# Kernel tuning notes

Measured on AMD Instinct MI355X. Metric: run time of the kernel, lower is better.

## Reference

```python
import jax, jax.numpy as jnp
import numpy as np

N_NODES = 100000
N_EDGES = 1600000
D_IN = 128
D_HID = 128
D_OUT = 2
N_GRAPHS = 64


def setup_inputs() -> dict:
    key = jax.random.key(0)
    ks = jax.random.split(key, 10)
    x = jax.random.normal(ks[0], (N_NODES, D_IN), dtype=jnp.float32)
    edge_index = jax.random.randint(ks[1], (2, N_EDGES), 0, N_NODES, dtype=jnp.int64)
    batch = jnp.sort(jax.random.randint(ks[2], (N_NODES,), 0, N_GRAPHS, dtype=jnp.int64))
    s_in = 1.0 / np.sqrt(D_IN)
    s_hid = 1.0 / np.sqrt(D_HID)
    W1 = jax.random.uniform(ks[3], (D_IN, D_HID), jnp.float32, -s_in, s_in)
    b1 = jnp.zeros((D_HID,), jnp.float32)
    W2 = jax.random.uniform(ks[4], (D_HID, D_HID), jnp.float32, -s_hid, s_hid)
    b2 = jnp.zeros((D_HID,), jnp.float32)
    W3 = jax.random.uniform(ks[5], (D_HID, D_OUT), jnp.float32, -s_hid, s_hid)
    b3 = jnp.zeros((D_OUT,), jnp.float32)
    return {"x": x, "edge_index": edge_index, "batch": batch,
            "W1": W1, "b1": b1, "W2": W2, "b2": b2, "W3": W3, "b3": b3}


def gcn_conv(x, W, b, src, dst, num_nodes):
    # PyG GCNConv: x' = D^{-1/2} (A + I) D^{-1/2} X W + b, edges flow src -> dst
    h = x @ W  # [N, F] transform first (smaller feature dim path)
    ones = jnp.ones((src.shape[0],), h.dtype)
    deg = jax.ops.segment_sum(ones, dst, num_segments=num_nodes) + 1.0  # self-loop
    dinv = jax.lax.rsqrt(deg)
    norm = dinv[src] * dinv[dst]  # per-edge symmetric normalization
    agg = jax.ops.segment_sum(h[src] * norm[:, None], dst, num_segments=num_nodes)
    out = agg + h * (dinv * dinv)[:, None]  # self-loop contribution
    return out + b


def reference(x, edge_index, batch, W1, b1, W2, b2, W3, b3):
    src, dst = edge_index[0], edge_index[1]
    n = x.shape[0]
    h = jax.nn.relu(gcn_conv(x, W1, b1, src, dst, n))   # dropout is identity in eval
    h = jax.nn.relu(gcn_conv(h, W2, b2, src, dst, n))
    h = gcn_conv(h, W3, b3, src, dst, n)
    # global mean pool over batch segments
    sums = jax.ops.segment_sum(h, batch, num_segments=N_GRAPHS)
    cnts = jax.ops.segment_sum(jnp.ones((n,), h.dtype), batch, num_segments=N_GRAPHS)
    return sums / jnp.maximum(cnts, 1.0)[:, None]
```

## Files before the change

### kernel.cpp

```cpp
#include <hip/hip_runtime.h>
#include <hip/hip_fp16.h>

#define EPB 8192
#define SEGCAP 12288

typedef __attribute__((ext_vector_type(8))) _Float16 half8;
typedef __attribute__((ext_vector_type(4))) float f32x4;
typedef __attribute__((ext_vector_type(4))) int i32x4;


__global__ void scan1(const int* __restrict__ v, int* __restrict__ incl,
                      int* __restrict__ bsum, int n) {
    __shared__ int tmp[256];
    int t = threadIdx.x;
    int gid = blockIdx.x * 256 + t;
    tmp[t] = (gid < n) ? v[gid] : 0;
    __syncthreads();
    for (int off = 1; off < 256; off <<= 1) {
        int x = (t >= off) ? tmp[t - off] : 0;
        __syncthreads();
        tmp[t] += x;
        __syncthreads();
    }
    if (gid < n) incl[gid] = tmp[t];
    if (t == 255) bsum[blockIdx.x] = tmp[255];
}

__global__ void scan2(const int* __restrict__ bsum, int* __restrict__ boff, int nb) {
    __shared__ int tmp[512];
    int t = threadIdx.x;
    int orig = (t < nb) ? bsum[t] : 0;
    tmp[t] = orig;
    __syncthreads();
    for (int off = 1; off < 512; off <<= 1) {
        int x = (t >= off) ? tmp[t - off] : 0;
        __syncthreads();
        tmp[t] += x;
        __syncthreads();
    }
    if (t < nb) boff[t] = tmp[t] - orig;
}

__global__ void basec_k(const int* __restrict__ incl, const int* __restrict__ boff,
                        const int* __restrict__ hist, int* __restrict__ base, int T) {
    int i = blockIdx.x * 256 + threadIdx.x;
    if (i < T) base[i] = incl[i] + boff[blockIdx.x] - hist[i];
}


__global__ __launch_bounds__(256) void hist_k(const int* __restrict__ dst,
                                              int* __restrict__ hist,
                                              int E, int nblk, int nbuk) {
    __shared__ int h[512];
    int t = threadIdx.x;
    for (int i = t; i < nbuk; i += 256) h[i] = 0;
    __syncthreads();
    int start = blockIdx.x * EPB;
    int end = start + EPB; if (end > E) end = E;
    if (end - start == EPB) {
        const i32x4* dv = (const i32x4*)(dst + start);
#pragma unroll
        for (int p = 0; p < 8; ++p) {
            i32x4 d4 = dv[t + p * 256];
            atomicAdd(&h[d4.x >> 8], 1);
            atomicAdd(&h[d4.y >> 8], 1);
            atomicAdd(&h[d4.z >> 8], 1);
            atomicAdd(&h[d4.w >> 8], 1);
        }
    } else {
        for (int e = start + t; e < end; e += 256) atomicAdd(&h[dst[e] >> 8], 1);
    }
    __syncthreads();
    for (int i = t; i < nbuk; i += 256) hist[i * nblk + blockIdx.x] = h[i];
}


__global__ __launch_bounds__(256) void binscatter_k(const int* __restrict__ src,
                                                    const int* __restrict__ dst,
                                                    const int* __restrict__ base,
                                                    unsigned int* __restrict__ binned,
                                                    int E, int nblk, int nbuk) {
    __shared__ int hloc[512];
    __shared__ int lstart[512];
    __shared__ int stmp[512];
    __shared__ unsigned int pk[EPB];
    __shared__ unsigned short bid[EPB];
    int t = threadIdx.x;
    int blk = blockIdx.x;
    int start = blk * EPB;
    int end = start + EPB; if (end > E) end = E;
    int cntE = end - start;

    for (int i = t; i < nbuk; i += 256) hloc[i] = 0;
    __syncthreads();
    for (int e = start + t; e < end; e += 256) atomicAdd(&hloc[dst[e] >> 8], 1);
    __syncthreads();
    for (int i = t; i < 512; i += 256) stmp[i] = (i < nbuk) ? hloc[i] : 0;
    __syncthreads();
    for (int off = 1; off < 512; off <<= 1) {
        int v0 = (t >= off) ? stmp[t - off] : 0;
        int v1 = stmp[t + 256 - off];
        __syncthreads();
        stmp[t] += v0;
        stmp[t + 256] += v1;
        __syncthreads();
    }
    for (int i = t; i < nbuk; i += 256) {
        int ex = stmp[i] - hloc[i];
        lstart[i] = ex;
        hloc[i] = ex;
    }
    __syncthreads();
    for (int e = start + t; e < end; e += 256) {
        int d = dst[e];
        int b = d >> 8;
        int r = atomicAdd(&hloc[b], 1);
        pk[r] = (unsigned int)src[e] | ((unsigned int)(d & 255) << 24);
        bid[r] = (unsigned short)b;
    }
    __syncthreads();
    for (int i = t; i < cntE; i += 256) {
        int b = bid[i];
        binned[base[b * nblk + blk] + (i - lstart[b])] = pk[i];
    }
}


__global__ __launch_bounds__(256) void group_k(const unsigned int* __restrict__ binned,
                                               const int* __restrict__ base,
                                               int* __restrict__ rowptr,
                                               float* __restrict__ dinv,
                                               int* __restrict__ col,
                                               int nblk, int nbuk, int N, int E) {
    __shared__ int cntL[256];
    __shared__ int sc[256];
    __shared__ int cur[256];
    __shared__ int stage[SEGCAP];
    int b = blockIdx.x, t = threadIdx.x;
    int segstart = base[b * nblk];
    int segend = (b + 1 < nbuk) ? base[(b + 1) * nblk] : E;
    int seglen = segend - segstart;

    cntL[t] = 0;
    __syncthreads();
    for (int i = segstart + t; i < segend; i += 256)
        atomicAdd(&cntL[binned[i] >> 24], 1);
    __syncthreads();
    sc[t] = cntL[t];
    __syncthreads();
    for (int off = 1; off < 256; off <<= 1) {
        int v = (t >= off) ? sc[t - off] : 0;
        __syncthreads();
        sc[t] += v;
        __syncthreads();
    }
    int n = (b << 8) + t;
    if (n < N) {
        rowptr[n + 1] = segstart + sc[t];
        dinv[n] = rsqrtf((float)cntL[t] + 1.0f);
    }
    if (b == 0 && t == 0) rowptr[0] = 0;
    cur[t] = sc[t] - cntL[t];
    __syncthreads();
    if (seglen <= SEGCAP) {
        for (int i = segstart + t; i < segend; i += 256) {
            unsigned int p = binned[i];
            int r = atomicAdd(&cur[p >> 24], 1);
            stage[r] = (int)(p & 0xFFFFFFu);
        }
        __syncthreads();
        for (int i = t; i < seglen; i += 256) col[segstart + i] = stage[i];
    } else {
        for (int i = segstart + t; i < segend; i += 256) {
            unsigned int p = binned[i];
            int r = atomicAdd(&cur[p >> 24], 1);
            col[segstart + r] = (int)(p & 0xFFFFFFu);
        }
    }
}


__global__ __launch_bounds__(256) void packW_k(const float* __restrict__ W,
                                               _Float16* __restrict__ Wp) {
    int t = blockIdx.x * 256 + threadIdx.x;
    int lane = t & 63, qct = t >> 6;
    int q = qct >> 3, ct = qct & 7;
    int krow = q * 32 + (lane >> 4) * 8;
    int c = ct * 16 + (lane & 15);
#pragma unroll
    for (int j = 0; j < 8; ++j)
        Wp[(size_t)t * 8 + j] = (_Float16)W[(krow + j) * 128 + c];
}


template<typename XT>
__global__ __launch_bounds__(256) void gemm_mfma(const XT* __restrict__ X,
                                                 const _Float16* __restrict__ Wp,
                                                 const float* __restrict__ dinv,
                                                 _Float16* __restrict__ Gh, int M) {
    constexpr bool F32 = (sizeof(XT) == 4);
    __shared__ _Float16 Wl[16384];
    int t = threadIdx.x;
    for (int i = t; i < 2048; i += 256)
        *(float4*)&Wl[(size_t)i * 8] = ((const float4*)Wp)[i];

    int wid = t >> 6, lane = t & 63;
    int row0 = blockIdx.x * 64 + wid * 16;
    int arow = row0 + (lane & 15); if (arow >= M) arow = M - 1;
    int kgrp = (lane >> 4) * 8;

    half8 a[4];
    if constexpr (F32) {
#pragma unroll
        for (int q = 0; q < 4; ++q) {
            const float* p = (const float*)X + (size_t)arow * 128 + q * 32 + kgrp;
            float4 u = *(const float4*)p;
            float4 v = *(const float4*)(p + 4);
            half8 h;
            h[0] = (_Float16)u.x; h[1] = (_Float16)u.y;
            h[2] = (_Float16)u.z; h[3] = (_Float16)u.w;
            h[4] = (_Float16)v.x; h[5] = (_Float16)v.y;
            h[6] = (_Float16)v.z; h[7] = (_Float16)v.w;
            a[q] = h;
        }
    } else {
#pragma unroll
        for (int q = 0; q < 4; ++q)
            a[q] = *(const half8*)((const _Float16*)X + (size_t)arow * 128 + q * 32 + kgrp);
    }
    __syncthreads();

    f32x4 acc[8];
#pragma unroll
    for (int ct = 0; ct < 8; ++ct) acc[ct] = (f32x4){0.f, 0.f, 0.f, 0.f};

#pragma unroll
    for (int q = 0; q < 4; ++q) {
#pragma unroll
        for (int ct = 0; ct < 8; ++ct) {
            half8 b = *(const half8*)&Wl[(size_t)((q * 8 + ct) * 64 + lane) * 8];
            acc[ct] = __builtin_amdgcn_mfma_f32_16x16x32_f16(a[q], b, acc[ct], 0, 0, 0);
        }
    }

    int rbase = row0 + (lane >> 4) * 4;
#pragma unroll
    for (int reg = 0; reg < 4; ++reg) {
        int r = rbase + reg;
        if (r < M) {
            float di = dinv[r];
#pragma unroll
            for (int ct = 0; ct < 8; ++ct)
                Gh[(size_t)r * 128 + ct * 16 + (lane & 15)] = (_Float16)(acc[ct][reg] * di);
        }
    }
}


__device__ __forceinline__ void addpk(__half2* acc, float4 v) {
    const __half2* h = reinterpret_cast<const __half2*>(&v);
#pragma unroll
    for (int j = 0; j < 4; ++j) acc[j] = __hadd2(acc[j], h[j]);
}

__global__ __launch_bounds__(256) void aggregate128h(const float4* __restrict__ G4,
                                                     const float* __restrict__ dinv,
                                                     const int* __restrict__ rowptr,
                                                     const int* __restrict__ col,
                                                     const float4* __restrict__ bias4,
                                                     float4* __restrict__ OutH, int N) {
    int n = blockIdx.x * 4 + (threadIdx.x >> 6);
    if (n >= N) return;
    int lane = threadIdx.x & 63;
    int f = lane & 15;
    int slot = lane >> 4;
    int e0 = rowptr[n], e1 = rowptr[n + 1];
    __half2 acc[4];
#pragma unroll
    for (int j = 0; j < 4; ++j) acc[j] = __float2half2_rn(0.f);

    int base = e0;
    for (; base + 16 <= e1; base += 16) {
        int s0 = col[base + slot];
        int s1 = col[base + 4 + slot];
        int s2 = col[base + 8 + slot];
        int s3 = col[base + 12 + slot];
        float4 v0 = G4[(size_t)s0 * 16 + f];
        float4 v1 = G4[(size_t)s1 * 16 + f];
        float4 v2 = G4[(size_t)s2 * 16 + f];
        float4 v3 = G4[(size_t)s3 * 16 + f];
        addpk(acc, v0); addpk(acc, v1); addpk(acc, v2); addpk(acc, v3);
    }
    for (int idx = base + slot; idx < e1; idx += 4) {
        float4 v = G4[(size_t)col[idx] * 16 + f];
        addpk(acc, v);
    }
    float a[8];
#pragma unroll
    for (int j = 0; j < 4; ++j) {
        float2 fp = __half22float2(acc[j]);
        a[2 * j] = fp.x;
        a[2 * j + 1] = fp.y;
    }
#pragma unroll
    for (int j = 0; j < 8; ++j) {
        a[j] += __shfl_xor(a[j], 16);
        a[j] += __shfl_xor(a[j], 32);
    }
    if (slot == 0) {
        float4 g = G4[(size_t)n * 16 + f];
        const __half2* sp = (const __half2*)&g;
        float di = dinv[n];
        float4 b0 = bias4[f * 2], b1 = bias4[f * 2 + 1];
        float o[8];
#pragma unroll
        for (int j = 0; j < 4; ++j) {
            float2 fp = __half22float2(sp[j]);
            o[2 * j]     = di * (a[2 * j] + fp.x);
            o[2 * j + 1] = di * (a[2 * j + 1] + fp.y);
        }
        o[0] += b0.x; o[1] += b0.y; o[2] += b0.z; o[3] += b0.w;
        o[4] += b1.x; o[5] += b1.y; o[6] += b1.z; o[7] += b1.w;
#pragma unroll
        for (int j = 0; j < 8; ++j) o[j] = fmaxf(o[j], 0.f);
        __half2 hh[4];
#pragma unroll
        for (int j = 0; j < 4; ++j) hh[j] = __floats2half2_rn(o[2 * j], o[2 * j + 1]);
        OutH[(size_t)n * 16 + f] = *(float4*)hh;
    }
}


__global__ __launch_bounds__(256) void aggregate128h_w3(const float4* __restrict__ G4,
                                                        const float* __restrict__ dinv,
                                                        const int* __restrict__ rowptr,
                                                        const int* __restrict__ col,
                                                        const float4* __restrict__ bias4,
                                                        const float* __restrict__ W3,
                                                        float* __restrict__ G3, int N) {
    int n = blockIdx.x * 4 + (threadIdx.x >> 6);
    if (n >= N) return;
    int lane = threadIdx.x & 63;
    int f = lane & 15;
    int slot = lane >> 4;
    int e0 = rowptr[n], e1 = rowptr[n + 1];
    __half2 acc[4];
#pragma unroll
    for (int j = 0; j < 4; ++j) acc[j] = __float2half2_rn(0.f);

    int base = e0;
    for (; base + 16 <= e1; base += 16) {
        int s0 = col[base + slot];
        int s1 = col[base + 4 + slot];
        int s2 = col[base + 8 + slot];
        int s3 = col[base + 12 + slot];
        float4 v0 = G4[(size_t)s0 * 16 + f];
        float4 v1 = G4[(size_t)s1 * 16 + f];
        float4 v2 = G4[(size_t)s2 * 16 + f];
        float4 v3 = G4[(size_t)s3 * 16 + f];
        addpk(acc, v0); addpk(acc, v1); addpk(acc, v2); addpk(acc, v3);
    }
    for (int idx = base + slot; idx < e1; idx += 4) {
        float4 v = G4[(size_t)col[idx] * 16 + f];
        addpk(acc, v);
    }
    float a[8];
#pragma unroll
    for (int j = 0; j < 4; ++j) {
        float2 fp = __half22float2(acc[j]);
        a[2 * j] = fp.x;
        a[2 * j + 1] = fp.y;
    }
#pragma unroll
    for (int j = 0; j < 8; ++j) {
        a[j] += __shfl_xor(a[j], 16);
        a[j] += __shfl_xor(a[j], 32);
    }
    float p0 = 0.f, p1 = 0.f;
    float di = dinv[n];
    if (slot == 0) {
        float4 g = G4[(size_t)n * 16 + f];
        const __half2* sp = (const __half2*)&g;
        float4 b0 = bias4[f * 2], b1 = bias4[f * 2 + 1];
        float o[8];
#pragma unroll
        for (int j = 0; j < 4; ++j) {
            float2 fp = __half22float2(sp[j]);
            o[2 * j]     = di * (a[2 * j] + fp.x);
            o[2 * j + 1] = di * (a[2 * j + 1] + fp.y);
        }
        o[0] += b0.x; o[1] += b0.y; o[2] += b0.z; o[3] += b0.w;
        o[4] += b1.x; o[5] += b1.y; o[6] += b1.z; o[7] += b1.w;
#pragma unroll
        for (int j = 0; j < 8; ++j) o[j] = fmaxf(o[j], 0.f);
        float w[16];
        *(float4*)&w[0]  = ((const float4*)W3)[f * 4 + 0];
        *(float4*)&w[4]  = ((const float4*)W3)[f * 4 + 1];
        *(float4*)&w[8]  = ((const float4*)W3)[f * 4 + 2];
        *(float4*)&w[12] = ((const float4*)W3)[f * 4 + 3];
#pragma unroll
        for (int j = 0; j < 8; ++j) {
            p0 += o[j] * w[2 * j];
            p1 += o[j] * w[2 * j + 1];
        }
    }
#pragma unroll
    for (int m = 1; m < 16; m <<= 1) {
        p0 += __shfl_xor(p0, m);
        p1 += __shfl_xor(p1, m);
    }
    if (lane == 0) {
        G3[(size_t)n * 2 + 0] = p0 * di;
        G3[(size_t)n * 2 + 1] = p1 * di;
    }
}


__global__ __launch_bounds__(256) void agg2pool(const float2* __restrict__ G3,
                                                const float* __restrict__ dinv,
                                                const int* __restrict__ rowptr,
                                                const int* __restrict__ col,
                                                const float* __restrict__ b3,
                                                const int* __restrict__ batch,
                                                float* __restrict__ pool, int N) {
    __shared__ float ls[192];
    for (int i = threadIdx.x; i < 192; i += 256) ls[i] = 0.f;
    __syncthreads();
    int n = blockIdx.x * 256 + threadIdx.x;
    if (n < N) {
        float s0 = 0.f, s1 = 0.f;
        int e0 = rowptr[n], e1 = rowptr[n + 1];
        int e = e0;
        for (; e + 4 <= e1; e += 4) {
            float2 v0 = G3[col[e]];
            float2 v1 = G3[col[e + 1]];
            float2 v2 = G3[col[e + 2]];
            float2 v3 = G3[col[e + 3]];
            s0 += v0.x + v1.x + v2.x + v3.x;
            s1 += v0.y + v1.y + v2.y + v3.y;
        }
        for (; e < e1; ++e) {
            float2 v = G3[col[e]];
            s0 += v.x; s1 += v.y;
        }
        float2 g = G3[n];
        float di = dinv[n];
        float o0 = di * (s0 + g.x) + b3[0];
        float o1 = di * (s1 + g.y) + b3[1];
        int gb = batch[n];
        atomicAdd(&ls[gb * 3 + 0], o0);
        atomicAdd(&ls[gb * 3 + 1], o1);
        atomicAdd(&ls[gb * 3 + 2], 1.0f);
    }
    __syncthreads();
    for (int i = threadIdx.x; i < 192; i += 256)
        if (ls[i] != 0.f) atomicAdd(&pool[i], ls[i]);
}

__global__ void finalize_k(const float* __restrict__ pool, float* __restrict__ out) {
    int t = threadIdx.x;
    if (t < 128) {
        int g = t >> 1, c = t & 1;
        out[t] = pool[g * 3 + c] / fmaxf(pool[g * 3 + 2], 1.0f);
    }
}


extern "C" void kernel_launch(void* const* d_in, const int* in_sizes, int n_in,
                              void* d_out, int out_size, void* d_ws, size_t ws_size,
                              hipStream_t stream) {
    const float* x   = (const float*)d_in[0];
    const int*  edge = (const int*)d_in[1];
    const int*  batch= (const int*)d_in[2];
    const float* W1  = (const float*)d_in[3];
    const float* b1  = (const float*)d_in[4];
    const float* W2  = (const float*)d_in[5];
    const float* b2  = (const float*)d_in[6];
    const float* W3  = (const float*)d_in[7];
    const float* b3  = (const float*)d_in[8];
    float* out = (float*)d_out;

    int N = in_sizes[0] / 128;
    int E = in_sizes[1] / 2;
    const int* src = edge;
    const int* dst = edge + E;

    int nblk1 = (E + EPB - 1) / EPB;
    int nbuk  = (N + 255) >> 8;
    int T     = nbuk * nblk1;
    int nb2   = (T + 255) / 256;

    char* base_ws = (char*)d_ws;
    size_t off = 0;
    auto alloc = [&](size_t bytes) -> void* {
        void* r = base_ws + off;
        off = (off + bytes + 255) & ~(size_t)255;
        return r;
    };
    _Float16*     GhA    = (_Float16*)alloc((size_t)N * 128 * 2);
    _Float16*     GhB    = (_Float16*)alloc((size_t)N * 128 * 2);
    _Float16*     Wp1    = (_Float16*)alloc(16384 * 2);
    _Float16*     Wp2    = (_Float16*)alloc(16384 * 2);
    float*        dinv   = (float*)alloc((size_t)N * 4);
    int*          rowptr = (int*)alloc((size_t)(N + 1) * 4);
    int*          col    = (int*)alloc((size_t)E * 4);
    unsigned int* binned = (unsigned int*)alloc((size_t)E * 4);
    int*          hist   = (int*)alloc((size_t)T * 4);
    int*          incl   = (int*)alloc((size_t)T * 4);
    int*          bsum   = (int*)alloc(1024 * 4);
    int*          boff   = (int*)alloc(1024 * 4);
    int*          basea  = (int*)alloc((size_t)(T + 1) * 4);
    float*        g3     = (float*)alloc((size_t)N * 2 * 4);
    float*        pool   = (float*)alloc(64 * 3 * 4);

    hipMemsetAsync(pool, 0, 64 * 3 * 4, stream);

    packW_k<<<8, 256, 0, stream>>>(W1, Wp1);
    packW_k<<<8, 256, 0, stream>>>(W2, Wp2);

    hist_k<<<nblk1, 256, 0, stream>>>(dst, hist, E, nblk1, nbuk);
    scan1<<<nb2, 256, 0, stream>>>(hist, incl, bsum, T);
    scan2<<<1, 512, 0, stream>>>(bsum, boff, nb2);
    basec_k<<<nb2, 256, 0, stream>>>(incl, boff, hist, basea, T);
    binscatter_k<<<nblk1, 256, 0, stream>>>(src, dst, basea, binned, E, nblk1, nbuk);
    group_k<<<nbuk, 256, 0, stream>>>(binned, basea, rowptr, dinv, col, nblk1, nbuk, N, E);

    int gb = (N + 63) / 64;
    int ab = (N + 3) / 4;

    gemm_mfma<float><<<gb, 256, 0, stream>>>(x, Wp1, dinv, GhA, N);
    aggregate128h<<<ab, 256, 0, stream>>>((const float4*)GhA, dinv, rowptr, col,
                                          (const float4*)b1, (float4*)GhB, N);
    gemm_mfma<_Float16><<<gb, 256, 0, stream>>>(GhB, Wp2, dinv, GhA, N);
    aggregate128h_w3<<<ab, 256, 0, stream>>>((const float4*)GhA, dinv, rowptr, col,
                                             (const float4*)b2, W3, g3, N);
    agg2pool<<<(N + 255) / 256, 256, 0, stream>>>((const float2*)g3, dinv, rowptr, col,
                                                  b3, batch, pool, N);
    finalize_k<<<1, 128, 0, stream>>>(pool, out);
}
```

Baseline: 233.0 us.

## Fuse layer-1 aggregation with layer-2 GEMM and halve edges per histogram block

Replaces the separate layer-1 aggregation kernel and layer-2 MFMA GEMM with one kernel. Each block aggregates 64 rows into LDS, then multiplies them by the packed W2 with MFMA, so the intermediate N×128 half tensor never round-trips through global memory. It also halves EPB, which doubles the number of histogram/binscatter blocks and widens scan2 to 1024 threads, and merges the two weight-pack launches into one. The cost is that each block now has only 4 wavefronts walking 16 nodes serially, so gather parallelism and occupancy are lower, and the block reads W2 fragments straight from global memory.

```diff
diff --git a/kernel.cpp b/kernel.cpp
--- a/kernel.cpp
+++ b/kernel.cpp
@@ -1,7 +1,7 @@
 #include <hip/hip_runtime.h>
 #include <hip/hip_fp16.h>
 
-#define EPB 8192
+#define EPB 4096
 #define SEGCAP 12288
 
 typedef __attribute__((ext_vector_type(8))) _Float16 half8;
@@ -27,12 +27,12 @@
 }
 
 __global__ void scan2(const int* __restrict__ bsum, int* __restrict__ boff, int nb) {
-    __shared__ int tmp[512];
+    __shared__ int tmp[1024];
     int t = threadIdx.x;
     int orig = (t < nb) ? bsum[t] : 0;
     tmp[t] = orig;
     __syncthreads();
-    for (int off = 1; off < 512; off <<= 1) {
+    for (int off = 1; off < 1024; off <<= 1) {
         int x = (t >= off) ? tmp[t - off] : 0;
         __syncthreads();
         tmp[t] += x;
@@ -60,7 +60,7 @@
     if (end - start == EPB) {
         const i32x4* dv = (const i32x4*)(dst + start);
 #pragma unroll
-        for (int p = 0; p < 8; ++p) {
+        for (int p = 0; p < EPB / 1024; ++p) {
             i32x4 d4 = dv[t + p * 256];
             atomicAdd(&h[d4.x >> 8], 1);
             atomicAdd(&h[d4.y >> 8], 1);
@@ -180,9 +180,13 @@
 }
 
 
-__global__ __launch_bounds__(256) void packW_k(const float* __restrict__ W,
-                                               _Float16* __restrict__ Wp) {
-    int t = blockIdx.x * 256 + threadIdx.x;
+__global__ __launch_bounds__(256) void packW2_k(const float* __restrict__ W1,
+                                                const float* __restrict__ W2,
+                                                _Float16* __restrict__ Wp1,
+                                                _Float16* __restrict__ Wp2) {
+    const float* W = (blockIdx.x < 8) ? W1 : W2;
+    _Float16* Wp = (blockIdx.x < 8) ? Wp1 : Wp2;
+    int t = (blockIdx.x & 7) * 256 + threadIdx.x;
     int lane = t & 63, qct = t >> 6;
     int q = qct >> 3, ct = qct & 7;
     int krow = q * 32 + (lane >> 4) * 8;
@@ -263,70 +267,109 @@
     for (int j = 0; j < 4; ++j) acc[j] = __hadd2(acc[j], h[j]);
 }
 
-__global__ __launch_bounds__(256) void aggregate128h(const float4* __restrict__ G4,
-                                                     const float* __restrict__ dinv,
-                                                     const int* __restrict__ rowptr,
-                                                     const int* __restrict__ col,
-                                                     const float4* __restrict__ bias4,
-                                                     float4* __restrict__ OutH, int N) {
-    int n = blockIdx.x * 4 + (threadIdx.x >> 6);
-    if (n >= N) return;
-    int lane = threadIdx.x & 63;
+
+__global__ __launch_bounds__(256) void agg_gemm(const float4* __restrict__ G4,
+                                                const float* __restrict__ dinv,
+                                                const int* __restrict__ rowptr,
+                                                const int* __restrict__ col,
+                                                const float4* __restrict__ bias4,
+                                                const _Float16* __restrict__ Wp,
+                                                _Float16* __restrict__ Gout, int N) {
+    __shared__ _Float16 Hl[64 * 136];
+    int t = threadIdx.x;
+    int wid = t >> 6, lane = t & 63;
     int f = lane & 15;
     int slot = lane >> 4;
-    int e0 = rowptr[n], e1 = rowptr[n + 1];
-    __half2 acc[4];
-#pragma unroll
-    for (int j = 0; j < 4; ++j) acc[j] = __float2half2_rn(0.f);
-
-    int base = e0;
-    for (; base + 16 <= e1; base += 16) {
-        int s0 = col[base + slot];
-        int s1 = col[base + 4 + slot];
-        int s2 = col[base + 8 + slot];
-        int s3 = col[base + 12 + slot];
-        float4 v0 = G4[(size_t)s0 * 16 + f];
-        float4 v1 = G4[(size_t)s1 * 16 + f];
-        float4 v2 = G4[(size_t)s2 * 16 + f];
-        float4 v3 = G4[(size_t)s3 * 16 + f];
-        addpk(acc, v0); addpk(acc, v1); addpk(acc, v2); addpk(acc, v3);
-    }
-    for (int idx = base + slot; idx < e1; idx += 4) {
-        float4 v = G4[(size_t)col[idx] * 16 + f];
-        addpk(acc, v);
-    }
-    float a[8];
-#pragma unroll
-    for (int j = 0; j < 4; ++j) {
-        float2 fp = __half22float2(acc[j]);
-        a[2 * j] = fp.x;
-        a[2 * j + 1] = fp.y;
-    }
-#pragma unroll
-    for (int j = 0; j < 8; ++j) {
-        a[j] += __shfl_xor(a[j], 16);
-        a[j] += __shfl_xor(a[j], 32);
-    }
-    if (slot == 0) {
-        float4 g = G4[(size_t)n * 16 + f];
-        const __half2* sp = (const __half2*)&g;
-        float di = dinv[n];
-        float4 b0 = bias4[f * 2], b1 = bias4[f * 2 + 1];
-        float o[8];
+    int row0 = blockIdx.x * 64;
+
+    for (int i = 0; i < 16; ++i) {
+        int n = row0 + wid * 16 + i;
+        if (n >= N) n = N - 1;
+        int e0 = rowptr[n], e1 = rowptr[n + 1];
+        __half2 acc[4];
+#pragma unroll
+        for (int j = 0; j < 4; ++j) acc[j] = __float2half2_rn(0.f);
+        int base = e0;
+        for (; base + 16 <= e1; base += 16) {
+            int s0 = col[base + slot];
+            int s1 = col[base + 4 + slot];
+            int s2 = col[base + 8 + slot];
+            int s3 = col[base + 12 + slot];
+            float4 v0 = G4[(size_t)s0 * 16 + f];
+            float4 v1 = G4[(size_t)s1 * 16 + f];
+            float4 v2 = G4[(size_t)s2 * 16 + f];
+            float4 v3 = G4[(size_t)s3 * 16 + f];
+            addpk(acc, v0); addpk(acc, v1); addpk(acc, v2); addpk(acc, v3);
+        }
+        for (int idx = base + slot; idx < e1; idx += 4) {
+            float4 v = G4[(size_t)col[idx] * 16 + f];
+            addpk(acc, v);
+        }
+        float a[8];
 #pragma unroll
         for (int j = 0; j < 4; ++j) {
-            float2 fp = __half22float2(sp[j]);
-            o[2 * j]     = di * (a[2 * j] + fp.x);
-            o[2 * j + 1] = di * (a[2 * j + 1] + fp.y);
-        }
-        o[0] += b0.x; o[1] += b0.y; o[2] += b0.z; o[3] += b0.w;
-        o[4] += b1.x; o[5] += b1.y; o[6] += b1.z; o[7] += b1.w;
-#pragma unroll
-        for (int j = 0; j < 8; ++j) o[j] = fmaxf(o[j], 0.f);
-        __half2 hh[4];
-#pragma unroll
-        for (int j = 0; j < 4; ++j) hh[j] = __floats2half2_rn(o[2 * j], o[2 * j + 1]);
-        OutH[(size_t)n * 16 + f] = *(float4*)hh;
+            float2 fp = __half22float2(acc[j]);
+            a[2 * j] = fp.x;
+            a[2 * j + 1] = fp.y;
+        }
+#pragma unroll
+        for (int j = 0; j < 8; ++j) {
+            a[j] += __shfl_xor(a[j], 16);
+            a[j] += __shfl_xor(a[j], 32);
+        }
+        if (slot == 0) {
+            float4 g = G4[(size_t)n * 16 + f];
+            const __half2* sp = (const __half2*)&g;
+            float di = dinv[n];
+            float4 b0 = bias4[f * 2], b1 = bias4[f * 2 + 1];
+            float o[8];
+#pragma unroll
+            for (int j = 0; j < 4; ++j) {
+                float2 fp = __half22float2(sp[j]);
+                o[2 * j]     = di * (a[2 * j] + fp.x);
+                o[2 * j + 1] = di * (a[2 * j + 1] + fp.y);
+            }
+            o[0] += b0.x; o[1] += b0.y; o[2] += b0.z; o[3] += b0.w;
+            o[4] += b1.x; o[5] += b1.y; o[6] += b1.z; o[7] += b1.w;
+#pragma unroll
+            for (int j = 0; j < 8; ++j) o[j] = fmaxf(o[j], 0.f);
+            __half2 hh[4];
+#pragma unroll
+            for (int j = 0; j < 4; ++j) hh[j] = __floats2half2_rn(o[2 * j], o[2 * j + 1]);
+            *(float4*)&Hl[(size_t)(wid * 16 + i) * 136 + f * 8] = *(float4*)hh;
+        }
+    }
+    __syncthreads();
+
+    int arowl = wid * 16 + (lane & 15);
+    int kgrp = (lane >> 4) * 8;
+    half8 av[4];
+#pragma unroll
+    for (int q = 0; q < 4; ++q)
+        av[q] = *(const half8*)&Hl[(size_t)arowl * 136 + q * 32 + kgrp];
+
+    f32x4 accm[8];
+#pragma unroll
+    for (int ct = 0; ct < 8; ++ct) accm[ct] = (f32x4){0.f, 0.f, 0.f, 0.f};
+#pragma unroll
+    for (int q = 0; q < 4; ++q) {
+#pragma unroll
+        for (int ct = 0; ct < 8; ++ct) {
+            half8 b = *(const half8*)&Wp[(size_t)((q * 8 + ct) * 64 + lane) * 8];
+            accm[ct] = __builtin_amdgcn_mfma_f32_16x16x32_f16(av[q], b, accm[ct], 0, 0, 0);
+        }
+    }
+    int rbase = row0 + wid * 16 + (lane >> 4) * 4;
+#pragma unroll
+    for (int reg = 0; reg < 4; ++reg) {
+        int r = rbase + reg;
+        if (r < N) {
+            float di = dinv[r];
+#pragma unroll
+            for (int ct = 0; ct < 8; ++ct)
+                Gout[(size_t)r * 128 + ct * 16 + (lane & 15)] =
+                    (_Float16)(accm[ct][reg] * di);
+        }
     }
 }
 
@@ -515,12 +558,11 @@
 
     hipMemsetAsync(pool, 0, 64 * 3 * 4, stream);
 
-    packW_k<<<8, 256, 0, stream>>>(W1, Wp1);
-    packW_k<<<8, 256, 0, stream>>>(W2, Wp2);
+    packW2_k<<<16, 256, 0, stream>>>(W1, W2, Wp1, Wp2);
 
     hist_k<<<nblk1, 256, 0, stream>>>(dst, hist, E, nblk1, nbuk);
     scan1<<<nb2, 256, 0, stream>>>(hist, incl, bsum, T);
-    scan2<<<1, 512, 0, stream>>>(bsum, boff, nb2);
+    scan2<<<1, 1024, 0, stream>>>(bsum, boff, nb2);
     basec_k<<<nb2, 256, 0, stream>>>(incl, boff, hist, basea, T);
     binscatter_k<<<nblk1, 256, 0, stream>>>(src, dst, basea, binned, E, nblk1, nbuk);
     group_k<<<nbuk, 256, 0, stream>>>(binned, basea, rowptr, dinv, col, nblk1, nbuk, N, E);
@@ -529,10 +571,9 @@
     int ab = (N + 3) / 4;
 
     gemm_mfma<float><<<gb, 256, 0, stream>>>(x, Wp1, dinv, GhA, N);
-    aggregate128h<<<ab, 256, 0, stream>>>((const float4*)GhA, dinv, rowptr, col,
-                                          (const float4*)b1, (float4*)GhB, N);
-    gemm_mfma<_Float16><<<gb, 256, 0, stream>>>(GhB, Wp2, dinv, GhA, N);
-    aggregate128h_w3<<<ab, 256, 0, stream>>>((const float4*)GhA, dinv, rowptr, col,
+    agg_gemm<<<gb, 256, 0, stream>>>((const float4*)GhA, dinv, rowptr, col,
+                                     (const float4*)b1, Wp2, GhB, N);
+    aggregate128h_w3<<<ab, 256, 0, stream>>>((const float4*)GhB, dinv, rowptr, col,
                                              (const float4*)b2, W3, g3, N);
     agg2pool<<<(N + 255) / 256, 256, 0, stream>>>((const float2*)g3, dinv, rowptr, col,
                                                   b3, batch, pool, N);
```

After: 252.1 us. 1.08x slower.
